# Kernel optimization log

Hardware: AMD Instinct MI355X
Metric: run time of the kernel (lower is better)

Reference implementation:

```python
import jax, jax.numpy as jnp
import numpy as np

S = 14          # grid size
L_COORD = 5.0
L_NOOBJ = 0.5
BATCH = 4096


def setup_inputs() -> dict:
    key = jax.random.key(0)
    k1, k2, k3 = jax.random.split(key, 3)
    shape = (BATCH, S, S, 30)
    # strictly positive values so sqrt(w), sqrt(h) are well defined (as assumed by the torch code)
    pred = jax.random.uniform(k1, shape, dtype=jnp.float32, minval=0.01, maxval=1.0)
    target = jax.random.uniform(k2, shape, dtype=jnp.float32, minval=0.01, maxval=1.0)
    has_obj = (jax.random.uniform(k3, (BATCH, S, S)) < 0.3).astype(jnp.float32)
    target = target.at[..., 4].set(has_obj)
    return {"pred_tensor": pred, "target_tensor": target}


def _yolo_loss(pred_tensor, target_tensor):
    N = pred_tensor.shape[0]
    dt = pred_tensor.dtype

    obj = (target_tensor[..., 4] > 0).astype(dt)      # [N,S,S]
    noobj = (target_tensor[..., 4] == 0).astype(dt)   # [N,S,S]

    # ---- no-object confidence loss (channels 4 and 9 in cells without objects) ----
    d4 = pred_tensor[..., 4] - target_tensor[..., 4]
    d9 = pred_tensor[..., 9] - target_tensor[..., 9]
    no_object_loss = jnp.sum(noobj * (d4 * d4 + d9 * d9))

    # ---- class prediction loss (channels 10:30 in object cells) ----
    dcls = pred_tensor[..., 10:] - target_tensor[..., 10:]
    class_loss = jnp.sum(obj[..., None] * dcls * dcls)

    # ---- per-cell best-IoU box selection (vectorized over all cells) ----
    pboxes = pred_tensor[..., :10].reshape(N, S, S, 2, 5)    # [N,S,S,2,5]
    tboxes = target_tensor[..., :10].reshape(N, S, S, 2, 5)
    p = pboxes[..., :4]                                      # [N,S,S,2,4]
    t = tboxes[..., 0, :4]                                   # target box of the cell [N,S,S,4]

    # [x,y,w,h] (center+size, xy in grid units) -> corner coords
    p1 = p[..., :2] / S - p[..., 2:] / 2                     # [N,S,S,2,2]
    p2 = p[..., :2] / S + p[..., 2:] / 2
    t1 = t[..., :2] / S - t[..., 2:] / 2                     # [N,S,S,2]
    t2 = t[..., :2] / S + t[..., 2:] / 2

    lt = jnp.maximum(p1, t1[..., None, :])
    rb = jnp.minimum(p2, t2[..., None, :])
    wh = jnp.maximum(rb - lt, 0.0)
    inter = wh[..., 0] * wh[..., 1]                          # [N,S,S,2]
    area_p = (p2[..., 0] - p1[..., 0]) * (p2[..., 1] - p1[..., 1])
    area_t = ((t2[..., 0] - t1[..., 0]) * (t2[..., 1] - t1[..., 1]))[..., None]
    iou = inter / (area_p + area_t - inter)                  # [N,S,S,2]

    # torch code: if IoU[0] > IoU[1] pick box 0 else box 1 (ties -> box 1)
    pick1 = iou[..., 0] <= iou[..., 1]                       # [N,S,S] bool
    p_sel = jnp.where(pick1[..., None], pboxes[..., 1, :], pboxes[..., 0, :])  # [N,S,S,5]
    t_sel = jnp.where(pick1[..., None], tboxes[..., 1, :], tboxes[..., 0, :])
    iou_best = jnp.where(pick1, iou[..., 1], iou[..., 0])    # [N,S,S]

    dxy = p_sel[..., :2] - t_sel[..., :2]
    dwh = jnp.sqrt(p_sel[..., 2:4]) - jnp.sqrt(t_sel[..., 2:4])
    reg_loss = jnp.sum(obj[..., None] * dxy * dxy) + jnp.sum(obj[..., None] * dwh * dwh)

    # ---- containing-object confidence loss: pred conf vs best IoU ----
    dconf = p_sel[..., 4] - iou_best
    contain_loss = jnp.sum(obj * dconf * dconf)

    total = L_NOOBJ * no_object_loss + class_loss + L_COORD * reg_loss + contain_loss
    return total / N


def reference(pred_tensor, target_tensor):
    return _yolo_loss(pred_tensor, target_tensor)
```

## Files before the change

### kernel.cpp

```cpp
#include <hip/hip_runtime.h>

#define SDIM 14
#define L_COORD 5.0f
#define L_NOOBJ 0.5f
#define BATCH 4096
#define CELLS (BATCH * SDIM * SDIM)
#define BLOCK 128
#define NBLOCKS (CELLS / BLOCK)
#define CELL_F 30
#define BLK_F (BLOCK * CELL_F)
#define BLK_F2 (BLK_F / 2)

#define PBOX 0
#define TBOX (BLOCK * 10)
#define DCLS (2 * BLOCK * 10)
#define WSUM (DCLS + BLOCK * 22)
#define LDS_FLOATS (WSUM + 2)

__global__ __launch_bounds__(BLOCK, 4) void yolo_partial(
    const float* __restrict__ pred, const float* __restrict__ targ,
    float* __restrict__ partial) {
    __shared__ float lds[LDS_FLOATS];

    const int tid = threadIdx.x;
    const size_t base = (size_t)blockIdx.x * BLK_F;
    const float* P = pred + base;
    const float* T = targ + base;

    float2 p2[15], t2[15];
#pragma unroll
    for (int j = 0; j < 15; ++j) {
        const int idx = tid + j * BLOCK;
        p2[j] = *reinterpret_cast<const float2*>(P + 2 * idx);
        t2[j] = *reinterpret_cast<const float2*>(T + 2 * idx);
    }

#pragma unroll
    for (int j = 0; j < 15; ++j) {
        const int idx = tid + j * BLOCK;
        const int cell = idx / 15;
        const int c = (idx % 15) * 2;
        if (c < 10) {
            *reinterpret_cast<float2*>(&lds[PBOX + cell * 10 + c]) = p2[j];
            *reinterpret_cast<float2*>(&lds[TBOX + cell * 10 + c]) = t2[j];
        } else {
            float2 d;
            d.x = p2[j].x - t2[j].x;
            d.y = p2[j].y - t2[j].y;
            *reinterpret_cast<float2*>(&lds[DCLS + cell * 22 + (c - 10)]) = d;
        }
    }
    __syncthreads();

    float Pb[10], Tb[10];
#pragma unroll
    for (int j = 0; j < 5; ++j) {
        const float2 a = *reinterpret_cast<const float2*>(&lds[PBOX + tid * 10 + 2 * j]);
        const float2 b = *reinterpret_cast<const float2*>(&lds[TBOX + tid * 10 + 2 * j]);
        Pb[2 * j] = a.x; Pb[2 * j + 1] = a.y;
        Tb[2 * j] = b.x; Tb[2 * j + 1] = b.y;
    }

    float cls = 0.0f;
#pragma unroll
    for (int j = 0; j < 10; ++j) {
        const float2 d = *reinterpret_cast<const float2*>(&lds[DCLS + tid * 22 + 2 * j]);
        cls += d.x * d.x;
        cls += d.y * d.y;
    }

    const float d4 = Pb[4] - Tb[4];
    const float d9 = Pb[9] - Tb[9];
    const float noobj_l = L_NOOBJ * (d4 * d4 + d9 * d9);

    const float invS = 1.0f / (float)SDIM;
    const float t1x = Tb[0] * invS - Tb[2] * 0.5f;
    const float t1y = Tb[1] * invS - Tb[3] * 0.5f;
    const float t2x = Tb[0] * invS + Tb[2] * 0.5f;
    const float t2y = Tb[1] * invS + Tb[3] * 0.5f;
    const float area_t = (t2x - t1x) * (t2y - t1y);

    float iou0 = 0.0f, iou1 = 0.0f;
#pragma unroll
    for (int k = 0; k < 2; ++k) {
        const float bx = Pb[5 * k + 0], by = Pb[5 * k + 1];
        const float bw = Pb[5 * k + 2], bh = Pb[5 * k + 3];
        const float p1x = bx * invS - bw * 0.5f;
        const float p1y = by * invS - bh * 0.5f;
        const float p2x = bx * invS + bw * 0.5f;
        const float p2y = by * invS + bh * 0.5f;
        const float ltx = fmaxf(p1x, t1x), lty = fmaxf(p1y, t1y);
        const float rbx = fminf(p2x, t2x), rby = fminf(p2y, t2y);
        const float wx = fmaxf(rbx - ltx, 0.0f);
        const float wy = fmaxf(rby - lty, 0.0f);
        const float inter = wx * wy;
        const float area_p = (p2x - p1x) * (p2y - p1y);
        const float v = inter / (area_p + area_t - inter);
        if (k == 0) iou0 = v; else iou1 = v;
    }

    const bool pick1 = (iou0 <= iou1);
    const float iou_best = pick1 ? iou1 : iou0;
    const float psx = pick1 ? Pb[5] : Pb[0];
    const float psy = pick1 ? Pb[6] : Pb[1];
    const float psw = pick1 ? Pb[7] : Pb[2];
    const float psh = pick1 ? Pb[8] : Pb[3];
    const float psc = pick1 ? Pb[9] : Pb[4];
    const float tsx = pick1 ? Tb[5] : Tb[0];
    const float tsy = pick1 ? Tb[6] : Tb[1];
    const float tsw = pick1 ? Tb[7] : Tb[2];
    const float tsh = pick1 ? Tb[8] : Tb[3];

    const float dx = psx - tsx, dy = psy - tsy;
    const float dw = sqrtf(psw) - sqrtf(tsw);
    const float dh = sqrtf(psh) - sqrtf(tsh);
    const float reg = dx * dx + dy * dy + dw * dw + dh * dh;
    const float dconf = psc - iou_best;
    const float obj_l = cls + L_COORD * reg + dconf * dconf;

    float loss = (Tb[4] > 0.0f) ? obj_l : noobj_l;

#pragma unroll
    for (int off = 32; off > 0; off >>= 1)
        loss += __shfl_down(loss, off, 64);

    const int lane = tid & 63;
    const int wave = tid >> 6;
    if (lane == 0) lds[WSUM + wave] = loss;
    __syncthreads();
    if (tid == 0)
        partial[blockIdx.x] = lds[WSUM + 0] + lds[WSUM + 1];
}

__global__ __launch_bounds__(256) void yolo_final(
    const float* __restrict__ partial, float* __restrict__ out) {
    float s = 0.0f;
    for (int i = threadIdx.x; i < NBLOCKS; i += 256) s += partial[i];
#pragma unroll
    for (int off = 32; off > 0; off >>= 1)
        s += __shfl_down(s, off, 64);
    __shared__ float wsum[256 / 64];
    const int lane = threadIdx.x & 63;
    const int wave = threadIdx.x >> 6;
    if (lane == 0) wsum[wave] = s;
    __syncthreads();
    if (threadIdx.x == 0)
        out[0] = (wsum[0] + wsum[1] + wsum[2] + wsum[3]) * (1.0f / (float)BATCH);
}

extern "C" void kernel_launch(void* const* d_in, const int* in_sizes, int n_in,
                              void* d_out, int out_size, void* d_ws, size_t ws_size,
                              hipStream_t stream) {
    const float* pred = (const float*)d_in[0];
    const float* targ = (const float*)d_in[1];
    float* out = (float*)d_out;
    float* partial = (float*)d_ws;

    yolo_partial<<<NBLOCKS, BLOCK, 0, stream>>>(pred, targ, partial);
    yolo_final<<<1, 256, 0, stream>>>(partial, out);
}
```

Before: 211.1 us.

## Process two tiles per block with register prefetch and in-register class loss

Each 256-thread block now handles two 256-cell tiles and issues the global loads for the second tile while the first is being computed. Class-difference squares are accumulated directly from registers, weighted by the object flag read from LDS, so the class region is no longer staged through shared memory. This cuts LDS traffic and the block count, and is meant to hide memory latency. The cost is higher register pressure (two sets of 15 float2 plus the diffs) and hand-written barriers using inline waitcnt.

```diff
diff --git a/kernel.cpp b/kernel.cpp
--- a/kernel.cpp
+++ b/kernel.cpp
@@ -3,139 +3,164 @@
 #define SDIM 14
 #define L_COORD 5.0f
 #define L_NOOBJ 0.5f
-#define BATCH 4096
-#define CELLS (BATCH * SDIM * SDIM)
-#define BLOCK 128
-#define NBLOCKS (CELLS / BLOCK)
+#define NIMG 4096
+#define CELLS (NIMG * SDIM * SDIM)
+#define BLOCK 256
+#define CPB BLOCK
+#define NTILE (CELLS / CPB)
+#define TPB 2
+#define GRID (NTILE / TPB)
 #define CELL_F 30
-#define BLK_F (BLOCK * CELL_F)
-#define BLK_F2 (BLK_F / 2)
+#define TILE_F (CPB * CELL_F)
 
 #define PBOX 0
-#define TBOX (BLOCK * 10)
-#define DCLS (2 * BLOCK * 10)
-#define WSUM (DCLS + BLOCK * 22)
-#define LDS_FLOATS (WSUM + 2)
+#define TBOX (CPB * 10)
+#define LDSF (2 * CPB * 10)
 
-__global__ __launch_bounds__(BLOCK, 4) void yolo_partial(
+__global__ __launch_bounds__(BLOCK, 3) void yolo_partial(
     const float* __restrict__ pred, const float* __restrict__ targ,
     float* __restrict__ partial) {
-    __shared__ float lds[LDS_FLOATS];
+    __shared__ float lds[LDSF];
+    __shared__ float wsum[BLOCK / 64];
+    const int tid = threadIdx.x;
+    const int tile0 = blockIdx.x * TPB;
 
-    const int tid = threadIdx.x;
-    const size_t base = (size_t)blockIdx.x * BLK_F;
-    const float* P = pred + base;
-    const float* T = targ + base;
+    float acc = 0.0f;
+    float2 p[15], t[15];
 
-    float2 p2[15], t2[15];
+    {
+        const float* P = pred + (size_t)tile0 * TILE_F;
+        const float* T = targ + (size_t)tile0 * TILE_F;
 #pragma unroll
-    for (int j = 0; j < 15; ++j) {
-        const int idx = tid + j * BLOCK;
-        p2[j] = *reinterpret_cast<const float2*>(P + 2 * idx);
-        t2[j] = *reinterpret_cast<const float2*>(T + 2 * idx);
+        for (int j = 0; j < 15; ++j) {
+            const int idx = tid + j * BLOCK;
+            p[j] = *reinterpret_cast<const float2*>(P + 2 * idx);
+            t[j] = *reinterpret_cast<const float2*>(T + 2 * idx);
+        }
     }
 
 #pragma unroll
-    for (int j = 0; j < 15; ++j) {
-        const int idx = tid + j * BLOCK;
-        const int cell = idx / 15;
-        const int c = (idx % 15) * 2;
-        if (c < 10) {
-            *reinterpret_cast<float2*>(&lds[PBOX + cell * 10 + c]) = p2[j];
-            *reinterpret_cast<float2*>(&lds[TBOX + cell * 10 + c]) = t2[j];
-        } else {
-            float2 d;
-            d.x = p2[j].x - t2[j].x;
-            d.y = p2[j].y - t2[j].y;
-            *reinterpret_cast<float2*>(&lds[DCLS + cell * 22 + (c - 10)]) = d;
+    for (int b = 0; b < TPB; ++b) {
+        float2 dif[15];
+#pragma unroll
+        for (int j = 0; j < 15; ++j) {
+            const int idx = tid + j * BLOCK;
+            const int cell = idx / 15;
+            const int pc = idx % 15;
+            if (pc < 5) {
+                *reinterpret_cast<float2*>(&lds[PBOX + cell * 10 + 2 * pc]) = p[j];
+                *reinterpret_cast<float2*>(&lds[TBOX + cell * 10 + 2 * pc]) = t[j];
+            } else {
+                dif[j].x = p[j].x - t[j].x;
+                dif[j].y = p[j].y - t[j].y;
+            }
         }
+
+        if (b + 1 < TPB) {
+            const float* P = pred + (size_t)(tile0 + b + 1) * TILE_F;
+            const float* T = targ + (size_t)(tile0 + b + 1) * TILE_F;
+#pragma unroll
+            for (int j = 0; j < 15; ++j) {
+                const int idx = tid + j * BLOCK;
+                p[j] = *reinterpret_cast<const float2*>(P + 2 * idx);
+                t[j] = *reinterpret_cast<const float2*>(T + 2 * idx);
+            }
+        }
+
+        asm volatile("s_waitcnt lgkmcnt(0)" ::: "memory");
+        __builtin_amdgcn_s_barrier();
+
+        float Pb[10], Tb[10];
+#pragma unroll
+        for (int c = 0; c < 10; c += 2) {
+            const float2 a = *reinterpret_cast<const float2*>(&lds[PBOX + tid * 10 + c]);
+            const float2 bb = *reinterpret_cast<const float2*>(&lds[TBOX + tid * 10 + c]);
+            Pb[c] = a.x; Pb[c + 1] = a.y;
+            Tb[c] = bb.x; Tb[c + 1] = bb.y;
+        }
+
+        const float d4 = Pb[4] - Tb[4];
+        const float d9 = Pb[9] - Tb[9];
+        const float noobj_l = L_NOOBJ * (d4 * d4 + d9 * d9);
+
+        const float invS = 1.0f / (float)SDIM;
+        const float t1x = Tb[0] * invS - Tb[2] * 0.5f;
+        const float t1y = Tb[1] * invS - Tb[3] * 0.5f;
+        const float t2x = Tb[0] * invS + Tb[2] * 0.5f;
+        const float t2y = Tb[1] * invS + Tb[3] * 0.5f;
+        const float area_t = (t2x - t1x) * (t2y - t1y);
+
+        float iou0 = 0.0f, iou1 = 0.0f;
+#pragma unroll
+        for (int k = 0; k < 2; ++k) {
+            const float bx = Pb[5 * k + 0], by = Pb[5 * k + 1];
+            const float bw = Pb[5 * k + 2], bh = Pb[5 * k + 3];
+            const float p1x = bx * invS - bw * 0.5f;
+            const float p1y = by * invS - bh * 0.5f;
+            const float p2x = bx * invS + bw * 0.5f;
+            const float p2y = by * invS + bh * 0.5f;
+            const float ltx = fmaxf(p1x, t1x), lty = fmaxf(p1y, t1y);
+            const float rbx = fminf(p2x, t2x), rby = fminf(p2y, t2y);
+            const float wx = fmaxf(rbx - ltx, 0.0f);
+            const float wy = fmaxf(rby - lty, 0.0f);
+            const float inter = wx * wy;
+            const float area_p = (p2x - p1x) * (p2y - p1y);
+            const float v = inter / (area_p + area_t - inter);
+            if (k == 0) iou0 = v; else iou1 = v;
+        }
+
+        const bool pick1 = (iou0 <= iou1);
+        const float iou_best = pick1 ? iou1 : iou0;
+        const float psx = pick1 ? Pb[5] : Pb[0];
+        const float psy = pick1 ? Pb[6] : Pb[1];
+        const float psw = pick1 ? Pb[7] : Pb[2];
+        const float psh = pick1 ? Pb[8] : Pb[3];
+        const float psc = pick1 ? Pb[9] : Pb[4];
+        const float tsx = pick1 ? Tb[5] : Tb[0];
+        const float tsy = pick1 ? Tb[6] : Tb[1];
+        const float tsw = pick1 ? Tb[7] : Tb[2];
+        const float tsh = pick1 ? Tb[8] : Tb[3];
+
+        const float dx = psx - tsx, dy = psy - tsy;
+        const float dw = sqrtf(psw) - sqrtf(tsw);
+        const float dh = sqrtf(psh) - sqrtf(tsh);
+        const float reg = dx * dx + dy * dy + dw * dw + dh * dh;
+        const float dconf = psc - iou_best;
+        const float obj_l = L_COORD * reg + dconf * dconf;
+
+        acc += (Tb[4] > 0.0f) ? obj_l : noobj_l;
+
+#pragma unroll
+        for (int j = 0; j < 15; ++j) {
+            const int idx = tid + j * BLOCK;
+            const int cell = idx / 15;
+            const int pc = idx % 15;
+            if (pc >= 5) {
+                const float obj = lds[TBOX + cell * 10 + 4];
+                acc += obj * (dif[j].x * dif[j].x);
+                acc += obj * (dif[j].y * dif[j].y);
+            }
+        }
+
+        asm volatile("s_waitcnt lgkmcnt(0)" ::: "memory");
+        __builtin_amdgcn_s_barrier();
     }
-    __syncthreads();
-
-    float Pb[10], Tb[10];
-#pragma unroll
-    for (int j = 0; j < 5; ++j) {
-        const float2 a = *reinterpret_cast<const float2*>(&lds[PBOX + tid * 10 + 2 * j]);
-        const float2 b = *reinterpret_cast<const float2*>(&lds[TBOX + tid * 10 + 2 * j]);
-        Pb[2 * j] = a.x; Pb[2 * j + 1] = a.y;
-        Tb[2 * j] = b.x; Tb[2 * j + 1] = b.y;
-    }
-
-    float cls = 0.0f;
-#pragma unroll
-    for (int j = 0; j < 10; ++j) {
-        const float2 d = *reinterpret_cast<const float2*>(&lds[DCLS + tid * 22 + 2 * j]);
-        cls += d.x * d.x;
-        cls += d.y * d.y;
-    }
-
-    const float d4 = Pb[4] - Tb[4];
-    const float d9 = Pb[9] - Tb[9];
-    const float noobj_l = L_NOOBJ * (d4 * d4 + d9 * d9);
-
-    const float invS = 1.0f / (float)SDIM;
-    const float t1x = Tb[0] * invS - Tb[2] * 0.5f;
-    const float t1y = Tb[1] * invS - Tb[3] * 0.5f;
-    const float t2x = Tb[0] * invS + Tb[2] * 0.5f;
-    const float t2y = Tb[1] * invS + Tb[3] * 0.5f;
-    const float area_t = (t2x - t1x) * (t2y - t1y);
-
-    float iou0 = 0.0f, iou1 = 0.0f;
-#pragma unroll
-    for (int k = 0; k < 2; ++k) {
-        const float bx = Pb[5 * k + 0], by = Pb[5 * k + 1];
-        const float bw = Pb[5 * k + 2], bh = Pb[5 * k + 3];
-        const float p1x = bx * invS - bw * 0.5f;
-        const float p1y = by * invS - bh * 0.5f;
-        const float p2x = bx * invS + bw * 0.5f;
-        const float p2y = by * invS + bh * 0.5f;
-        const float ltx = fmaxf(p1x, t1x), lty = fmaxf(p1y, t1y);
-        const float rbx = fminf(p2x, t2x), rby = fminf(p2y, t2y);
-        const float wx = fmaxf(rbx - ltx, 0.0f);
-        const float wy = fmaxf(rby - lty, 0.0f);
-        const float inter = wx * wy;
-        const float area_p = (p2x - p1x) * (p2y - p1y);
-        const float v = inter / (area_p + area_t - inter);
-        if (k == 0) iou0 = v; else iou1 = v;
-    }
-
-    const bool pick1 = (iou0 <= iou1);
-    const float iou_best = pick1 ? iou1 : iou0;
-    const float psx = pick1 ? Pb[5] : Pb[0];
-    const float psy = pick1 ? Pb[6] : Pb[1];
-    const float psw = pick1 ? Pb[7] : Pb[2];
-    const float psh = pick1 ? Pb[8] : Pb[3];
-    const float psc = pick1 ? Pb[9] : Pb[4];
-    const float tsx = pick1 ? Tb[5] : Tb[0];
-    const float tsy = pick1 ? Tb[6] : Tb[1];
-    const float tsw = pick1 ? Tb[7] : Tb[2];
-    const float tsh = pick1 ? Tb[8] : Tb[3];
-
-    const float dx = psx - tsx, dy = psy - tsy;
-    const float dw = sqrtf(psw) - sqrtf(tsw);
-    const float dh = sqrtf(psh) - sqrtf(tsh);
-    const float reg = dx * dx + dy * dy + dw * dw + dh * dh;
-    const float dconf = psc - iou_best;
-    const float obj_l = cls + L_COORD * reg + dconf * dconf;
-
-    float loss = (Tb[4] > 0.0f) ? obj_l : noobj_l;
 
 #pragma unroll
     for (int off = 32; off > 0; off >>= 1)
-        loss += __shfl_down(loss, off, 64);
-
+        acc += __shfl_down(acc, off, 64);
     const int lane = tid & 63;
     const int wave = tid >> 6;
-    if (lane == 0) lds[WSUM + wave] = loss;
+    if (lane == 0) wsum[wave] = acc;
     __syncthreads();
     if (tid == 0)
-        partial[blockIdx.x] = lds[WSUM + 0] + lds[WSUM + 1];
+        partial[blockIdx.x] = wsum[0] + wsum[1] + wsum[2] + wsum[3];
 }
 
 __global__ __launch_bounds__(256) void yolo_final(
     const float* __restrict__ partial, float* __restrict__ out) {
     float s = 0.0f;
-    for (int i = threadIdx.x; i < NBLOCKS; i += 256) s += partial[i];
+    for (int i = threadIdx.x; i < GRID; i += 256) s += partial[i];
 #pragma unroll
     for (int off = 32; off > 0; off >>= 1)
         s += __shfl_down(s, off, 64);
@@ -145,7 +170,7 @@
     if (lane == 0) wsum[wave] = s;
     __syncthreads();
     if (threadIdx.x == 0)
-        out[0] = (wsum[0] + wsum[1] + wsum[2] + wsum[3]) * (1.0f / (float)BATCH);
+        out[0] = (wsum[0] + wsum[1] + wsum[2] + wsum[3]) * (1.0f / (float)NIMG);
 }
 
 extern "C" void kernel_launch(void* const* d_in, const int* in_sizes, int n_in,
@@ -156,6 +181,6 @@
     float* out = (float*)d_out;
     float* partial = (float*)d_ws;
 
-    yolo_partial<<<NBLOCKS, BLOCK, 0, stream>>>(pred, targ, partial);
+    yolo_partial<<<GRID, BLOCK, 0, stream>>>(pred, targ, partial);
     yolo_final<<<1, 256, 0, stream>>>(partial, out);
 }
```

Result: no change. 211.1 us (+0.0%).
